# Optimization experiments

Measured on AMD Instinct MI355X. Metric: run time of the kernel, lower is better.

## Reference

```python
import jax, jax.numpy as jnp
import numpy as np
import math

B, L, C = 1, 4096, 1024
H = 16
D = C // H  # head_dim = 64


def setup_inputs() -> dict:
    key = jax.random.key(0)
    ks = jax.random.split(key, 5)
    s = 1.0 / math.sqrt(C)
    return {
        "x": jax.random.normal(ks[0], (B, L, C), dtype=jnp.float32),
        "Wq": jax.random.normal(ks[1], (C, C), dtype=jnp.float32) * s,
        "Wk": jax.random.normal(ks[2], (C, C), dtype=jnp.float32) * s,
        "Wv": jax.random.normal(ks[3], (C, C), dtype=jnp.float32) * s,
        "Wo": jax.random.normal(ks[4], (C, C), dtype=jnp.float32) * s,
    }


def reference(x, Wq, Wk, Wv, Wo):
    # Projections (bias=False). Wq etc. are applied as x @ W (equivalent
    # parameterization to torch Linear's x @ W.T with transposed storage).
    q = (x @ Wq).reshape(B, L, H, D).transpose(0, 2, 1, 3)  # (B,H,L,D)
    k = (x @ Wk).reshape(B, L, H, D).transpose(0, 2, 1, 3)
    v = (x @ Wv).reshape(B, L, H, D).transpose(0, 2, 1, 3)

    scale = 1.0 / math.sqrt(D)
    scores = jnp.einsum("bhqd,bhkd->bhqk", q, k) * scale  # (B,H,L,L)
    causal = jnp.tril(jnp.ones((L, L), dtype=bool))
    scores = jnp.where(causal[None, None, :, :], scores, -jnp.inf)
    probs = jax.nn.softmax(scores, axis=-1)  # dropout p=0 -> identity

    out = jnp.einsum("bhqk,bhkd->bhqd", probs, v)  # (B,H,L,D)
    out = out.transpose(0, 2, 1, 3).reshape(B, L, C)
    return out @ Wo  # resid dropout p=0 -> identity
```

## Files before the change

kernel.cpp:

```cpp
#include <hip/hip_runtime.h>

#define L_SEQ 4096
#define C_DIM 1024
#define H_NUM 16
#define D_HEAD 64
#define LDQKV 3072

typedef __bf16 bf16x8 __attribute__((ext_vector_type(8)));
typedef __bf16 bf16x4 __attribute__((ext_vector_type(4)));
typedef float f32x4 __attribute__((ext_vector_type(4)));

#define AS1 __attribute__((address_space(1)))
#define AS3 __attribute__((address_space(3)))

__device__ inline __bf16 f2bf(float f) {
  unsigned u = __builtin_bit_cast(unsigned, f);
  u = (u + 0x7fffu + ((u >> 16) & 1u)) >> 16;
  unsigned short s = (unsigned short)u;
  return __builtin_bit_cast(__bf16, s);
}

__device__ inline void gload_lds16(const __bf16* g, __bf16* l) {
  __builtin_amdgcn_global_load_lds((const AS1 void*)g, (AS3 void*)l, 16, 0, 0);
}

__global__ __launch_bounds__(256) void cvt_f32_bf16(const float* __restrict__ in,
                                                    __bf16* __restrict__ out) {
  int i = (blockIdx.x * 256 + threadIdx.x) * 4;
  float4 v = *(const float4*)(in + i);
  bf16x4 o = {f2bf(v.x), f2bf(v.y), f2bf(v.z), f2bf(v.w)};
  *(bf16x4*)(out + i) = o;
}

__global__ __launch_bounds__(256) void transpose_cvt(const float* __restrict__ W,
                                                     __bf16* __restrict__ Wt) {
  __shared__ float t[32][33];
  const int tx = threadIdx.x, ty = threadIdx.y;
  const int c0 = blockIdx.x * 32, r0 = blockIdx.y * 32;
#pragma unroll
  for (int k = 0; k < 4; ++k)
    t[ty + k * 8][tx] = W[(size_t)(r0 + ty + k * 8) * C_DIM + c0 + tx];
  __syncthreads();
#pragma unroll
  for (int k = 0; k < 4; ++k)
    Wt[(size_t)(c0 + ty + k * 8) * C_DIM + r0 + tx] = f2bf(t[tx][ty + k * 8]);
}

__global__ __launch_bounds__(256) void transpose_v(const __bf16* __restrict__ QKV,
                                                   __bf16* __restrict__ Vt) {
  __shared__ __bf16 t[32][34];
  const int tx = threadIdx.x, ty = threadIdx.y;
  const int q0 = blockIdx.x * 32, c0 = blockIdx.y * 32;
#pragma unroll
  for (int k = 0; k < 4; ++k)
    t[ty + k * 8][tx] = QKV[(size_t)(q0 + ty + k * 8) * LDQKV + 2048 + c0 + tx];
  __syncthreads();
#pragma unroll
  for (int k = 0; k < 4; ++k)
    Vt[(size_t)(c0 + ty + k * 8) * L_SEQ + q0 + tx] = t[tx][ty + k * 8];
}

template <bool OUT_BF16>
__global__ __launch_bounds__(256) void gemm_bt(const __bf16* __restrict__ A,
                                               const __bf16* __restrict__ Bt,
                                               void* __restrict__ Cp,
                                               int M, int N, int K) {
  __shared__ __bf16 As[128 * 32];
  __shared__ __bf16 Bs[128 * 32];
  const int tid = threadIdx.x;
  const int lane = tid & 63;
  const int wave = tid >> 6;
  const int wm = wave >> 1, wn = wave & 1;
  const int c16 = lane & 15, g4 = lane >> 4;
  const int srow = lane >> 2, scol = (lane & 3) * 8;

  f32x4 acc[4][4] = {};

  const size_t arow0 = (size_t)blockIdx.x * 128;
  const size_t brow0 = (size_t)blockIdx.y * 128;

  for (int kt = 0; kt < K; kt += 32) {
#pragma unroll
    for (int i = 0; i < 2; ++i) {
      const int row = i * 64 + wave * 16 + srow;
      gload_lds16(A + (arow0 + row) * K + kt + scol, As + (i * 64 + wave * 16) * 32);
      gload_lds16(Bt + (brow0 + row) * K + kt + scol, Bs + (i * 64 + wave * 16) * 32);
    }
    __syncthreads();
    bf16x8 af[4], bfr[4];
#pragma unroll
    for (int mi = 0; mi < 4; ++mi)
      af[mi] = *(const bf16x8*)(As + (wm * 64 + mi * 16 + c16) * 32 + g4 * 8);
#pragma unroll
    for (int ni = 0; ni < 4; ++ni)
      bfr[ni] = *(const bf16x8*)(Bs + (wn * 64 + ni * 16 + c16) * 32 + g4 * 8);
#pragma unroll
    for (int mi = 0; mi < 4; ++mi)
#pragma unroll
      for (int ni = 0; ni < 4; ++ni)
        acc[mi][ni] = __builtin_amdgcn_mfma_f32_16x16x32_bf16(af[mi], bfr[ni], acc[mi][ni], 0, 0, 0);
    __syncthreads();
  }

#pragma unroll
  for (int mi = 0; mi < 4; ++mi)
#pragma unroll
    for (int ni = 0; ni < 4; ++ni)
#pragma unroll
      for (int i = 0; i < 4; ++i) {
        size_t row = arow0 + wm * 64 + mi * 16 + g4 * 4 + i;
        size_t col = brow0 + wn * 64 + ni * 16 + c16;
        if (OUT_BF16)
          ((__bf16*)Cp)[row * N + col] = f2bf(acc[mi][ni][i]);
        else
          ((float*)Cp)[row * N + col] = acc[mi][ni][i];
      }
}

__global__ __launch_bounds__(256) void attn_fwd(const __bf16* __restrict__ Q,
                                                const __bf16* __restrict__ Kg,
                                                const __bf16* __restrict__ Vt,
                                                __bf16* __restrict__ O) {
  const int bid = blockIdx.x;
  const int h = bid & 15;
  const int p = bid >> 4;
  const int qt0 = 63 - p, qt1 = p;

  __shared__ __bf16 Ks[2][64 * 64];
  __shared__ __bf16 Vs[2][64 * 64];
  __shared__ __bf16 Ps[4][16 * 64];

  const int tid = threadIdx.x;
  const int lane = tid & 63;
  const int wave = tid >> 6;
  const int c16 = lane & 15, g4 = lane >> 4;
  constexpr float SC = 0.125f * 1.44269504088896f;

  const int rl = lane >> 3;
  const int cs = (lane & 7) ^ rl;

  auto stage = [&](int kv, int b) {
#pragma unroll
    for (int i = 0; i < 2; ++i) {
      const int r = (i * 4 + wave) * 8 + rl;
      gload_lds16(Kg + (size_t)(kv * 64 + r) * LDQKV + h * D_HEAD + cs * 8,
                  &Ks[b][(i * 4 + wave) * 512]);
      gload_lds16(Vt + (size_t)(h * D_HEAD + r) * L_SEQ + kv * 64 + cs * 8,
                  &Vs[b][(i * 4 + wave) * 512]);
    }
  };

  int cur = 0;
  stage(0, 0);

#pragma unroll
  for (int seg = 0; seg < 2; ++seg) {
    const int qtc = seg ? qt1 : qt0;
    const int qrow0 = qtc * 64 + wave * 16;

    const __bf16* qp = Q + (size_t)(qrow0 + c16) * LDQKV + h * D_HEAD + g4 * 8;
    bf16x8 qa0 = *(const bf16x8*)qp;
    bf16x8 qa1 = *(const bf16x8*)(qp + 32);

    f32x4 acc[4] = {};
    float mrow[4], lrow[4];
#pragma unroll
    for (int i = 0; i < 4; ++i) { mrow[i] = -1e30f; lrow[i] = 0.f; }

    for (int kv = 0; kv <= qtc; ++kv) {
      const bool have_next = (kv < qtc) || (seg == 0);
      if (have_next) {
        stage((kv < qtc) ? kv + 1 : 0, cur ^ 1);
        asm volatile("s_waitcnt vmcnt(4)" ::: "memory");
      } else {
        asm volatile("s_waitcnt vmcnt(0)" ::: "memory");
      }
      __builtin_amdgcn_sched_barrier(0);
      __builtin_amdgcn_s_barrier();
      __builtin_amdgcn_sched_barrier(0);

      char* const KsB = (char*)&Ks[cur][0];
      char* const VsB = (char*)&Vs[cur][0];
      const int kv0 = kv * 64;

      f32x4 s[4];
      __builtin_amdgcn_s_setprio(1);
#pragma unroll
      for (int n = 0; n < 4; ++n) {
        const int row = n * 16 + c16;
        const int rb = row * 128;
        const int x7 = row & 7;
        bf16x8 k0 = *(const bf16x8*)(KsB + rb + ((g4 ^ x7) << 4));
        bf16x8 k1 = *(const bf16x8*)(KsB + rb + (((4 + g4) ^ x7) << 4));
        f32x4 z = {};
        z = __builtin_amdgcn_mfma_f32_16x16x32_bf16(qa0, k0, z, 0, 0, 0);
        z = __builtin_amdgcn_mfma_f32_16x16x32_bf16(qa1, k1, z, 0, 0, 0);
        s[n] = z;
      }
      __builtin_amdgcn_s_setprio(0);

      if (kv == qtc) {
#pragma unroll
        for (int n = 0; n < 4; ++n) {
          const int key = kv0 + n * 16 + c16;
#pragma unroll
          for (int i = 0; i < 4; ++i) {
            const int q = qrow0 + g4 * 4 + i;
            s[n][i] = (key <= q) ? s[n][i] * SC : -1e30f;
          }
        }
      } else {
#pragma unroll
        for (int n = 0; n < 4; ++n)
#pragma unroll
          for (int i = 0; i < 4; ++i) s[n][i] *= SC;
      }

      float corr[4];
#pragma unroll
      for (int i = 0; i < 4; ++i) {
        float v = fmaxf(fmaxf(s[0][i], s[1][i]), fmaxf(s[2][i], s[3][i]));
        v = fmaxf(v, __shfl_xor(v, 1, 64));
        v = fmaxf(v, __shfl_xor(v, 2, 64));
        v = fmaxf(v, __shfl_xor(v, 4, 64));
        v = fmaxf(v, __shfl_xor(v, 8, 64));
        const float mnew = fmaxf(mrow[i], v);
        corr[i] = exp2f(mrow[i] - mnew);
        mrow[i] = mnew;
      }
      float rs[4] = {0.f, 0.f, 0.f, 0.f};
#pragma unroll
      for (int n = 0; n < 4; ++n)
#pragma unroll
        for (int i = 0; i < 4; ++i) {
          const float pv = exp2f(s[n][i] - mrow[i]);
          s[n][i] = pv;
          rs[i] += pv;
        }
#pragma unroll
      for (int i = 0; i < 4; ++i) {
        float v = rs[i];
        v += __shfl_xor(v, 1, 64);
        v += __shfl_xor(v, 2, 64);
        v += __shfl_xor(v, 4, 64);
        v += __shfl_xor(v, 8, 64);
        lrow[i] = lrow[i] * corr[i] + v;
      }
#pragma unroll
      for (int n = 0; n < 4; ++n)
#pragma unroll
        for (int i = 0; i < 4; ++i) acc[n][i] *= corr[i];

      char* const pw = (char*)&Ps[wave][0];
#pragma unroll
      for (int n = 0; n < 4; ++n) {
        const int ch = n * 2 + (c16 >> 3);
#pragma unroll
        for (int i = 0; i < 4; ++i) {
          const int row = g4 * 4 + i;
          *(__bf16*)(pw + row * 128 + ((ch ^ (row & 7)) << 4) + (c16 & 7) * 2) =
              f2bf(s[n][i]);
        }
      }
      asm volatile("s_waitcnt lgkmcnt(0)" ::: "memory");
      __builtin_amdgcn_sched_barrier(0);

      __builtin_amdgcn_s_setprio(1);
#pragma unroll
      for (int kh = 0; kh < 2; ++kh) {
        const int chk = kh * 4 + g4;
        bf16x8 pa = *(const bf16x8*)(pw + c16 * 128 + ((chk ^ (c16 & 7)) << 4));
#pragma unroll
        for (int n = 0; n < 4; ++n) {
          const int row = n * 16 + c16;
          bf16x8 vb = *(const bf16x8*)(VsB + row * 128 + ((chk ^ (row & 7)) << 4));
          acc[n] = __builtin_amdgcn_mfma_f32_16x16x32_bf16(pa, vb, acc[n], 0, 0, 0);
        }
      }
      __builtin_amdgcn_s_setprio(0);

      __builtin_amdgcn_sched_barrier(0);
      __builtin_amdgcn_s_barrier();
      __builtin_amdgcn_sched_barrier(0);
      cur ^= 1;
    }

#pragma unroll
    for (int n = 0; n < 4; ++n)
#pragma unroll
      for (int i = 0; i < 4; ++i) {
        const int q = qrow0 + g4 * 4 + i;
        O[(size_t)q * C_DIM + h * D_HEAD + n * 16 + c16] = f2bf(acc[n][i] / lrow[i]);
      }
  }
}

extern "C" void kernel_launch(void* const* d_in, const int* in_sizes, int n_in,
                              void* d_out, int out_size, void* d_ws, size_t ws_size,
                              hipStream_t stream) {
  const float* x = (const float*)d_in[0];
  const float* Wq = (const float*)d_in[1];
  const float* Wk = (const float*)d_in[2];
  const float* Wv = (const float*)d_in[3];
  const float* Wo = (const float*)d_in[4];
  float* out = (float*)d_out;

  char* ws = (char*)d_ws;
  __bf16* xb    = (__bf16*)(ws);
  __bf16* WqkvT = (__bf16*)(ws + (8u << 20));
  __bf16* WoT   = (__bf16*)(ws + (14u << 20));
  __bf16* QKVb  = (__bf16*)(ws + (16u << 20));
  __bf16* Vtb   = (__bf16*)(ws + (40u << 20));
  __bf16* Ab    = xb;

  cvt_f32_bf16<<<4096, 256, 0, stream>>>(x, xb);

  dim3 tb(32, 8);
  dim3 tg(32, 32);
  transpose_cvt<<<tg, tb, 0, stream>>>(Wq, WqkvT);
  transpose_cvt<<<tg, tb, 0, stream>>>(Wk, WqkvT + (size_t)1024 * 1024);
  transpose_cvt<<<tg, tb, 0, stream>>>(Wv, WqkvT + (size_t)2048 * 1024);
  transpose_cvt<<<tg, tb, 0, stream>>>(Wo, WoT);

  gemm_bt<true><<<dim3(L_SEQ / 128, LDQKV / 128), 256, 0, stream>>>(
      xb, WqkvT, QKVb, L_SEQ, LDQKV, C_DIM);

  transpose_v<<<dim3(L_SEQ / 32, C_DIM / 32), tb, 0, stream>>>(QKVb, Vtb);

  attn_fwd<<<512, 256, 0, stream>>>(QKVb, QKVb + 1024, Vtb, Ab);

  gemm_bt<false><<<dim3(L_SEQ / 128, C_DIM / 128), 256, 0, stream>>>(
      Ab, WoT, out, L_SEQ, C_DIM, C_DIM);
}
```

Before: 287.9 us.

## Rewrite attention with 32x32 MFMA, register-resident P, folded softmax scale

```diff
diff --git a/kernel.cpp b/kernel.cpp
--- a/kernel.cpp
+++ b/kernel.cpp
@@ -9,9 +9,14 @@
 typedef __bf16 bf16x8 __attribute__((ext_vector_type(8)));
 typedef __bf16 bf16x4 __attribute__((ext_vector_type(4)));
 typedef float f32x4 __attribute__((ext_vector_type(4)));
+typedef float f32x16 __attribute__((ext_vector_type(16)));
+typedef unsigned int u32;
+typedef u32 u32x4 __attribute__((ext_vector_type(4)));
 
 #define AS1 __attribute__((address_space(1)))
 #define AS3 __attribute__((address_space(3)))
+
+#define SC_LOG2E 0.1803368801111204f
 
 __device__ inline __bf16 f2bf(float f) {
   unsigned u = __builtin_bit_cast(unsigned, f);
@@ -32,9 +37,15 @@
   *(bf16x4*)(out + i) = o;
 }
 
-__global__ __launch_bounds__(256) void transpose_cvt(const float* __restrict__ W,
-                                                     __bf16* __restrict__ Wt) {
+__global__ __launch_bounds__(256) void transpose_cvt4(const float* __restrict__ W0,
+                                                      const float* __restrict__ W1,
+                                                      const float* __restrict__ W2,
+                                                      const float* __restrict__ W3,
+                                                      __bf16* __restrict__ dst) {
   __shared__ float t[32][33];
+  const int z = blockIdx.z;
+  const float* W = (z == 0) ? W0 : (z == 1) ? W1 : (z == 2) ? W2 : W3;
+  __bf16* Wt = dst + (size_t)z * 1048576;
   const int tx = threadIdx.x, ty = threadIdx.y;
   const int c0 = blockIdx.x * 32, r0 = blockIdx.y * 32;
 #pragma unroll
@@ -64,7 +75,8 @@
 __global__ __launch_bounds__(256) void gemm_bt(const __bf16* __restrict__ A,
                                                const __bf16* __restrict__ Bt,
                                                void* __restrict__ Cp,
-                                               int M, int N, int K) {
+                                               int M, int N, int K,
+                                               float cscale, int scale_ncols) {
   __shared__ __bf16 As[128 * 32];
   __shared__ __bf16 Bs[128 * 32];
   const int tid = threadIdx.x;
@@ -102,6 +114,7 @@
     __syncthreads();
   }
 
+  const float esc = ((int)brow0 < scale_ncols) ? cscale : 1.0f;
 #pragma unroll
   for (int mi = 0; mi < 4; ++mi)
 #pragma unroll
@@ -111,30 +124,32 @@
         size_t row = arow0 + wm * 64 + mi * 16 + g4 * 4 + i;
         size_t col = brow0 + wn * 64 + ni * 16 + c16;
         if (OUT_BF16)
-          ((__bf16*)Cp)[row * N + col] = f2bf(acc[mi][ni][i]);
+          ((__bf16*)Cp)[row * N + col] = f2bf(acc[mi][ni][i] * esc);
         else
           ((float*)Cp)[row * N + col] = acc[mi][ni][i];
       }
 }
 
-__global__ __launch_bounds__(256) void attn_fwd(const __bf16* __restrict__ Q,
-                                                const __bf16* __restrict__ Kg,
-                                                const __bf16* __restrict__ Vt,
-                                                __bf16* __restrict__ O) {
+__global__ __launch_bounds__(256, 2) void attn_fwd(const __bf16* __restrict__ Q,
+                                                   const __bf16* __restrict__ Kg,
+                                                   const __bf16* __restrict__ Vt,
+                                                   __bf16* __restrict__ O) {
   const int bid = blockIdx.x;
   const int h = bid & 15;
-  const int p = bid >> 4;
-  const int qt0 = 63 - p, qt1 = p;
+  const int qt = 31 - (bid >> 4);
+  const int nt = 2 * qt + 2;
 
   __shared__ __bf16 Ks[2][64 * 64];
   __shared__ __bf16 Vs[2][64 * 64];
-  __shared__ __bf16 Ps[4][16 * 64];
 
   const int tid = threadIdx.x;
   const int lane = tid & 63;
   const int wave = tid >> 6;
-  const int c16 = lane & 15, g4 = lane >> 4;
-  constexpr float SC = 0.125f * 1.44269504088896f;
+  const int l31 = lane & 31;
+  const int hl = lane >> 5;
+  const int qbase = qt * 128 + wave * 32;
+  const int q = qbase + l31;
+  const int kvmax_w = (qbase + 31) >> 6;
 
   const int rl = lane >> 3;
   const int cs = (lane & 7) ^ rl;
@@ -150,148 +165,150 @@
     }
   };
 
+  stage(0, 0);
+
+  bf16x8 qf[4];
+  {
+    const __bf16* qp = Q + (size_t)q * LDQKV + h * D_HEAD + hl * 8;
+#pragma unroll
+    for (int s = 0; s < 4; ++s) qf[s] = *(const bf16x8*)(qp + s * 16);
+  }
+
+  f32x16 acc0 = {}, acc1 = {};
+  float m = -1e30f, lsum = 0.f;
+
   int cur = 0;
-  stage(0, 0);
-
-#pragma unroll
-  for (int seg = 0; seg < 2; ++seg) {
-    const int qtc = seg ? qt1 : qt0;
-    const int qrow0 = qtc * 64 + wave * 16;
-
-    const __bf16* qp = Q + (size_t)(qrow0 + c16) * LDQKV + h * D_HEAD + g4 * 8;
-    bf16x8 qa0 = *(const bf16x8*)qp;
-    bf16x8 qa1 = *(const bf16x8*)(qp + 32);
-
-    f32x4 acc[4] = {};
-    float mrow[4], lrow[4];
-#pragma unroll
-    for (int i = 0; i < 4; ++i) { mrow[i] = -1e30f; lrow[i] = 0.f; }
-
-    for (int kv = 0; kv <= qtc; ++kv) {
-      const bool have_next = (kv < qtc) || (seg == 0);
-      if (have_next) {
-        stage((kv < qtc) ? kv + 1 : 0, cur ^ 1);
-        asm volatile("s_waitcnt vmcnt(4)" ::: "memory");
-      } else {
-        asm volatile("s_waitcnt vmcnt(0)" ::: "memory");
-      }
-      __builtin_amdgcn_sched_barrier(0);
-      __builtin_amdgcn_s_barrier();
-      __builtin_amdgcn_sched_barrier(0);
-
+  for (int kv = 0; kv < nt; ++kv) {
+    if (kv + 1 < nt) {
+      stage(kv + 1, cur ^ 1);
+      asm volatile("s_waitcnt vmcnt(4)" ::: "memory");
+    } else {
+      asm volatile("s_waitcnt vmcnt(0)" ::: "memory");
+    }
+    __builtin_amdgcn_sched_barrier(0);
+    __builtin_amdgcn_s_barrier();
+    __builtin_amdgcn_sched_barrier(0);
+
+    if (kv <= kvmax_w) {
       char* const KsB = (char*)&Ks[cur][0];
       char* const VsB = (char*)&Vs[cur][0];
-      const int kv0 = kv * 64;
-
-      f32x4 s[4];
+
+      f32x16 st0 = {}, st1 = {};
       __builtin_amdgcn_s_setprio(1);
 #pragma unroll
-      for (int n = 0; n < 4; ++n) {
-        const int row = n * 16 + c16;
-        const int rb = row * 128;
-        const int x7 = row & 7;
-        bf16x8 k0 = *(const bf16x8*)(KsB + rb + ((g4 ^ x7) << 4));
-        bf16x8 k1 = *(const bf16x8*)(KsB + rb + (((4 + g4) ^ x7) << 4));
-        f32x4 z = {};
-        z = __builtin_amdgcn_mfma_f32_16x16x32_bf16(qa0, k0, z, 0, 0, 0);
-        z = __builtin_amdgcn_mfma_f32_16x16x32_bf16(qa1, k1, z, 0, 0, 0);
-        s[n] = z;
+      for (int s = 0; s < 4; ++s) {
+        const int ch = s * 2 + hl;
+        bf16x8 a0 = *(const bf16x8*)(KsB + l31 * 128 + ((ch ^ (l31 & 7)) << 4));
+        bf16x8 a1 = *(const bf16x8*)(KsB + (32 + l31) * 128 + ((ch ^ (l31 & 7)) << 4));
+        st0 = __builtin_amdgcn_mfma_f32_32x32x16_bf16(a0, qf[s], st0, 0, 0, 0);
+        st1 = __builtin_amdgcn_mfma_f32_32x32x16_bf16(a1, qf[s], st1, 0, 0, 0);
       }
       __builtin_amdgcn_s_setprio(0);
 
-      if (kv == qtc) {
-#pragma unroll
-        for (int n = 0; n < 4; ++n) {
-          const int key = kv0 + n * 16 + c16;
-#pragma unroll
-          for (int i = 0; i < 4; ++i) {
-            const int q = qrow0 + g4 * 4 + i;
-            s[n][i] = (key <= q) ? s[n][i] * SC : -1e30f;
-          }
+      if (kv == kvmax_w) {
+#pragma unroll
+        for (int r = 0; r < 16; ++r) {
+          const int kr = (r & 3) + 8 * (r >> 2) + 4 * hl;
+          const int k0 = kv * 64 + kr;
+          st0[r] = (k0 <= q) ? st0[r] : -1e30f;
+          st1[r] = (k0 + 32 <= q) ? st1[r] : -1e30f;
         }
-      } else {
-#pragma unroll
-        for (int n = 0; n < 4; ++n)
-#pragma unroll
-          for (int i = 0; i < 4; ++i) s[n][i] *= SC;
-      }
-
-      float corr[4];
-#pragma unroll
-      for (int i = 0; i < 4; ++i) {
-        float v = fmaxf(fmaxf(s[0][i], s[1][i]), fmaxf(s[2][i], s[3][i]));
-        v = fmaxf(v, __shfl_xor(v, 1, 64));
-        v = fmaxf(v, __shfl_xor(v, 2, 64));
-        v = fmaxf(v, __shfl_xor(v, 4, 64));
-        v = fmaxf(v, __shfl_xor(v, 8, 64));
-        const float mnew = fmaxf(mrow[i], v);
-        corr[i] = exp2f(mrow[i] - mnew);
-        mrow[i] = mnew;
-      }
-      float rs[4] = {0.f, 0.f, 0.f, 0.f};
-#pragma unroll
-      for (int n = 0; n < 4; ++n)
-#pragma unroll
-        for (int i = 0; i < 4; ++i) {
-          const float pv = exp2f(s[n][i] - mrow[i]);
-          s[n][i] = pv;
-          rs[i] += pv;
-        }
-#pragma unroll
-      for (int i = 0; i < 4; ++i) {
-        float v = rs[i];
-        v += __shfl_xor(v, 1, 64);
-        v += __shfl_xor(v, 2, 64);
-        v += __shfl_xor(v, 4, 64);
-        v += __shfl_xor(v, 8, 64);
-        lrow[i] = lrow[i] * corr[i] + v;
-      }
-#pragma unroll
-      for (int n = 0; n < 4; ++n)
-#pragma unroll
-        for (int i = 0; i < 4; ++i) acc[n][i] *= corr[i];
-
-      char* const pw = (char*)&Ps[wave][0];
-#pragma unroll
-      for (int n = 0; n < 4; ++n) {
-        const int ch = n * 2 + (c16 >> 3);
-#pragma unroll
-        for (int i = 0; i < 4; ++i) {
-          const int row = g4 * 4 + i;
-          *(__bf16*)(pw + row * 128 + ((ch ^ (row & 7)) << 4) + (c16 & 7) * 2) =
-              f2bf(s[n][i]);
-        }
-      }
-      asm volatile("s_waitcnt lgkmcnt(0)" ::: "memory");
-      __builtin_amdgcn_sched_barrier(0);
+      }
+
+      float t[16];
+#pragma unroll
+      for (int r = 0; r < 16; ++r) t[r] = fmaxf(st0[r], st1[r]);
+#pragma unroll
+      for (int w = 8; w > 0; w >>= 1)
+#pragma unroll
+        for (int r = 0; r < w; ++r) t[r] = fmaxf(t[r], t[r + w]);
+      float mx = fmaxf(t[0], __shfl_xor(t[0], 32, 64));
+      const float mnew = fmaxf(m, mx);
+      const float corr = exp2f(m - mnew);
+      m = mnew;
+
+#pragma unroll
+      for (int r = 0; r < 16; ++r) {
+        st0[r] = exp2f(st0[r] - m);
+        st1[r] = exp2f(st1[r] - m);
+      }
+      float sm[16];
+#pragma unroll
+      for (int r = 0; r < 16; ++r) sm[r] = st0[r] + st1[r];
+#pragma unroll
+      for (int w = 8; w > 0; w >>= 1)
+#pragma unroll
+        for (int r = 0; r < w; ++r) sm[r] = sm[r] + sm[r + w];
+      float sl = sm[0] + __shfl_xor(sm[0], 32, 64);
+      lsum = lsum * corr + sl;
+      acc0 *= corr;
+      acc1 *= corr;
+
+      u32 w0[8], w1[8];
+#pragma unroll
+      for (int i = 0; i < 8; ++i) {
+        asm("v_cvt_pk_bf16_f32 %0, %1, %2" : "=v"(w0[i]) : "v"(st0[2 * i]), "v"(st0[2 * i + 1]));
+        asm("v_cvt_pk_bf16_f32 %0, %1, %2" : "=v"(w1[i]) : "v"(st1[2 * i]), "v"(st1[2 * i + 1]));
+      }
+      u32 e0a = (u32)__shfl_xor((int)(hl ? w0[0] : w0[2]), 32, 64);
+      u32 e0b = (u32)__shfl_xor((int)(hl ? w0[1] : w0[3]), 32, 64);
+      u32 e0c = (u32)__shfl_xor((int)(hl ? w0[4] : w0[6]), 32, 64);
+      u32 e0d = (u32)__shfl_xor((int)(hl ? w0[5] : w0[7]), 32, 64);
+      u32 e1a = (u32)__shfl_xor((int)(hl ? w1[0] : w1[2]), 32, 64);
+      u32 e1b = (u32)__shfl_xor((int)(hl ? w1[1] : w1[3]), 32, 64);
+      u32 e1c = (u32)__shfl_xor((int)(hl ? w1[4] : w1[6]), 32, 64);
+      u32 e1d = (u32)__shfl_xor((int)(hl ? w1[5] : w1[7]), 32, 64);
+      u32x4 f0 = hl ? (u32x4){e0a, e0b, w0[2], w0[3]} : (u32x4){w0[0], w0[1], e0a, e0b};
+      u32x4 f1 = hl ? (u32x4){e0c, e0d, w0[6], w0[7]} : (u32x4){w0[4], w0[5], e0c, e0d};
+      u32x4 f2 = hl ? (u32x4){e1a, e1b, w1[2], w1[3]} : (u32x4){w1[0], w1[1], e1a, e1b};
+      u32x4 f3 = hl ? (u32x4){e1c, e1d, w1[6], w1[7]} : (u32x4){w1[4], w1[5], e1c, e1d};
+      bf16x8 pb0 = __builtin_bit_cast(bf16x8, f0);
+      bf16x8 pb1 = __builtin_bit_cast(bf16x8, f1);
+      bf16x8 pb2 = __builtin_bit_cast(bf16x8, f2);
+      bf16x8 pb3 = __builtin_bit_cast(bf16x8, f3);
 
       __builtin_amdgcn_s_setprio(1);
 #pragma unroll
-      for (int kh = 0; kh < 2; ++kh) {
-        const int chk = kh * 4 + g4;
-        bf16x8 pa = *(const bf16x8*)(pw + c16 * 128 + ((chk ^ (c16 & 7)) << 4));
-#pragma unroll
-        for (int n = 0; n < 4; ++n) {
-          const int row = n * 16 + c16;
-          bf16x8 vb = *(const bf16x8*)(VsB + row * 128 + ((chk ^ (row & 7)) << 4));
-          acc[n] = __builtin_amdgcn_mfma_f32_16x16x32_bf16(pa, vb, acc[n], 0, 0, 0);
-        }
+      for (int s = 0; s < 4; ++s) {
+        const bf16x8 pb = (s == 0) ? pb0 : (s == 1) ? pb1 : (s == 2) ? pb2 : pb3;
+        const int ch = s * 2 + hl;
+        bf16x8 va0 = *(const bf16x8*)(VsB + l31 * 128 + ((ch ^ (l31 & 7)) << 4));
+        bf16x8 va1 = *(const bf16x8*)(VsB + (32 + l31) * 128 + ((ch ^ (l31 & 7)) << 4));
+        acc0 = __builtin_amdgcn_mfma_f32_32x32x16_bf16(va0, pb, acc0, 0, 0, 0);
+        acc1 = __builtin_amdgcn_mfma_f32_32x32x16_bf16(va1, pb, acc1, 0, 0, 0);
       }
       __builtin_amdgcn_s_setprio(0);
-
-      __builtin_amdgcn_sched_barrier(0);
-      __builtin_amdgcn_s_barrier();
-      __builtin_amdgcn_sched_barrier(0);
-      cur ^= 1;
-    }
-
-#pragma unroll
-    for (int n = 0; n < 4; ++n)
-#pragma unroll
-      for (int i = 0; i < 4; ++i) {
-        const int q = qrow0 + g4 * 4 + i;
-        O[(size_t)q * C_DIM + h * D_HEAD + n * 16 + c16] = f2bf(acc[n][i] / lrow[i]);
-      }
+    }
+
+    __builtin_amdgcn_sched_barrier(0);
+    __builtin_amdgcn_s_barrier();
+    __builtin_amdgcn_sched_barrier(0);
+    cur ^= 1;
+  }
+
+  const float rinv = 1.0f / lsum;
+  char* const Po = (char*)&Ks[0][0] + wave * 4096;
+#pragma unroll
+  for (int dt = 0; dt < 2; ++dt) {
+#pragma unroll
+    for (int i = 0; i < 8; ++i) {
+      const int r = 2 * i;
+      const int d = dt * 32 + (r & 3) + 8 * (r >> 2) + 4 * hl;
+      float lo = (dt ? acc1[r] : acc0[r]) * rinv;
+      float hi = (dt ? acc1[r + 1] : acc0[r + 1]) * rinv;
+      u32 wv;
+      asm("v_cvt_pk_bf16_f32 %0, %1, %2" : "=v"(wv) : "v"(lo), "v"(hi));
+      *(u32*)(Po + l31 * 128 + (((d >> 3) ^ (l31 & 7)) << 4) + (d & 7) * 2) = wv;
+    }
+  }
+  asm volatile("s_waitcnt lgkmcnt(0)" ::: "memory");
+  __builtin_amdgcn_sched_barrier(0);
+#pragma unroll
+  for (int j = 0; j < 4; ++j) {
+    const int qr = lane >> 1;
+    const int c = (lane & 1) * 4 + j;
+    bf16x8 ov = *(const bf16x8*)(Po + qr * 128 + ((c ^ (qr & 7)) << 4));
+    *(bf16x8*)(O + (size_t)(qbase + qr) * C_DIM + h * D_HEAD + c * 8) = ov;
   }
 }
 
@@ -308,27 +325,22 @@
   char* ws = (char*)d_ws;
   __bf16* xb    = (__bf16*)(ws);
   __bf16* WqkvT = (__bf16*)(ws + (8u << 20));
-  __bf16* WoT   = (__bf16*)(ws + (14u << 20));
   __bf16* QKVb  = (__bf16*)(ws + (16u << 20));
   __bf16* Vtb   = (__bf16*)(ws + (40u << 20));
+  __bf16* WoT   = WqkvT + (size_t)3 * 1048576;
   __bf16* Ab    = xb;
 
   cvt_f32_bf16<<<4096, 256, 0, stream>>>(x, xb);
 
-  dim3 tb(32, 8);
-  dim3 tg(32, 32);
-  transpose_cvt<<<tg, tb, 0, stream>>>(Wq, WqkvT);
-  transpose_cvt<<<tg, tb, 0, stream>>>(Wk, WqkvT + (size_t)1024 * 1024);
-  transpose_cvt<<<tg, tb, 0, stream>>>(Wv, WqkvT + (size_t)2048 * 1024);
-  transpose_cvt<<<tg, tb, 0, stream>>>(Wo, WoT);
+  transpose_cvt4<<<dim3(32, 32, 4), dim3(32, 8), 0, stream>>>(Wq, Wk, Wv, Wo, WqkvT);
 
   gemm_bt<true><<<dim3(L_SEQ / 128, LDQKV / 128), 256, 0, stream>>>(
-      xb, WqkvT, QKVb, L_SEQ, LDQKV, C_DIM);
-
-  transpose_v<<<dim3(L_SEQ / 32, C_DIM / 32), tb, 0, stream>>>(QKVb, Vtb);
+      xb, WqkvT, QKVb, L_SEQ, LDQKV, C_DIM, SC_LOG2E, 1024);
+
+  transpose_v<<<dim3(L_SEQ / 32, C_DIM / 32), dim3(32, 8), 0, stream>>>(QKVb, Vtb);
 
   attn_fwd<<<512, 256, 0, stream>>>(QKVb, QKVb + 1024, Vtb, Ab);
 
   gemm_bt<false><<<dim3(L_SEQ / 128, C_DIM / 128), 256, 0, stream>>>(
-      Ab, WoT, out, L_SEQ, C_DIM, C_DIM);
-}
+      Ab, WoT, out, L_SEQ, C_DIM, C_DIM, 1.0f, 0);
+}
```

Measured after the change: 258.6 us. -10.2%, faster.
